# Kernel optimization log

Hardware: AMD Instinct MI355X
Metric: run time of the kernel (lower is better)

Reference implementation:

```python
import jax, jax.numpy as jnp
import numpy as np

T, B, E, H = 2048, 2, 1024, 16
HD = E // H
EPS = 1e-5


def setup_inputs() -> dict:
    key = jax.random.key(0)
    k1, k2, k3 = jax.random.split(key, 3)
    bound_in = float(np.sqrt(6.0 / (3 * E + E)))   # xavier_uniform for [3E,E]
    bound_out = float(np.sqrt(6.0 / (E + E)))      # xavier_uniform for [E,E]
    return {
        "query": jax.random.normal(k1, (T, B, E), dtype=jnp.float32),
        "gamma": jnp.ones((E,), dtype=jnp.float32),
        "beta": jnp.zeros((E,), dtype=jnp.float32),
        "in_proj_weight": jax.random.uniform(k2, (3 * E, E), jnp.float32, -bound_in, bound_in),
        "out_proj_weight": jax.random.uniform(k3, (E, E), jnp.float32, -bound_out, bound_out),
    }


def reference(query, gamma, beta, in_proj_weight, out_proj_weight):
    # LayerNorm over channel dim
    mean = jnp.mean(query, axis=-1, keepdims=True)
    var = jnp.mean(jnp.square(query - mean), axis=-1, keepdims=True)
    ln = (query - mean) * jax.lax.rsqrt(var + EPS) * gamma + beta  # [T,B,E]

    # Fused QKV projection (no bias): qkv = ln @ W^T, W: [3E, E]
    qkv = jnp.einsum("tbe,fe->tbf", ln, in_proj_weight)  # [T,B,3E]
    q, k, v = jnp.split(qkv, 3, axis=-1)
    q = q.reshape(T, B, H, HD) * (HD ** -0.5)
    k = k.reshape(T, B, H, HD)
    v = v.reshape(T, B, H, HD)

    # Attention: scores [B,H,T,T]
    scores = jnp.einsum("tbhd,sbhd->bhts", q, k)
    attn = jax.nn.softmax(scores, axis=-1)
    ctx = jnp.einsum("bhts,sbhd->tbhd", attn, v).reshape(T, B, E)

    # Output projection + residual add (dropout prob = 0)
    out = jnp.einsum("tbe,fe->tbf", ctx, out_proj_weight)
    return query + out
```

## Files before the change

### kernel.cpp

```cpp
#include <hip/hip_runtime.h>
#include <hip/hip_bf16.h>
#include <math.h>

#define T_DIM 2048
#define B_DIM 2
#define E_DIM 1024
#define H_DIM 16
#define HD_DIM 64
#define M_DIM (T_DIM * B_DIM)
#define BH_DIM (B_DIM * H_DIM)

using bf16x8 = __attribute__((ext_vector_type(8))) __bf16;
using u16x8  = __attribute__((ext_vector_type(8))) unsigned short;
using f32x4  = __attribute__((ext_vector_type(4))) float;

static __device__ __forceinline__ unsigned short f2bf(float f) {
  unsigned u = __builtin_bit_cast(unsigned, f);
  u += 0x7fff + ((u >> 16) & 1);
  return (unsigned short)(u >> 16);
}

__device__ __forceinline__ void gload_lds16(const void* g, void* l) {
  __builtin_amdgcn_global_load_lds(
      (const __attribute__((address_space(1))) unsigned int*)g,
      (__attribute__((address_space(3))) unsigned int*)l, 16, 0, 0);
}

__global__ __launch_bounds__(256) void prep_kernel(
    const float* __restrict__ q, const float* __restrict__ gamma,
    const float* __restrict__ beta, unsigned short* __restrict__ ln_out,
    const float* __restrict__ w1, unsigned short* __restrict__ o1, int n1,
    const float* __restrict__ w2, unsigned short* __restrict__ o2, int n2) {
  int blk = blockIdx.x;
  int tid = threadIdx.x;
  if (blk >= M_DIM) {
    int i = (blk - M_DIM) * 256 + tid;
    const float* in; unsigned short* out; int idx;
    if (i < n1) { in = w1; out = o1; idx = i; }
    else if (i < n1 + n2) { in = w2; out = o2; idx = i - n1; }
    else return;
    float4 v = ((const float4*)in)[idx];
    ushort4 o;
    o.x = f2bf(v.x); o.y = f2bf(v.y); o.z = f2bf(v.z); o.w = f2bf(v.w);
    ((ushort4*)out)[idx] = o;
    return;
  }
  int row = blk;
  const float4* qr = (const float4*)(q + (size_t)row * E_DIM);
  float4 x = qr[tid];
  float s  = x.x + x.y + x.z + x.w;
  float ss = x.x * x.x + x.y * x.y + x.z * x.z + x.w * x.w;
#pragma unroll
  for (int off = 32; off >= 1; off >>= 1) {
    s  += __shfl_xor(s, off, 64);
    ss += __shfl_xor(ss, off, 64);
  }
  __shared__ float red[8];
  int wid = tid >> 6, lane = tid & 63;
  if (lane == 0) { red[wid] = s; red[4 + wid] = ss; }
  __syncthreads();
  s  = red[0] + red[1] + red[2] + red[3];
  ss = red[4] + red[5] + red[6] + red[7];
  float mean = s * (1.0f / E_DIM);
  float var  = ss * (1.0f / E_DIM) - mean * mean;
  float rstd = rsqrtf(var + 1e-5f);
  float4 g4 = ((const float4*)gamma)[tid];
  float4 b4 = ((const float4*)beta)[tid];
  ushort4 o;
  o.x = f2bf((x.x - mean) * rstd * g4.x + b4.x);
  o.y = f2bf((x.y - mean) * rstd * g4.y + b4.y);
  o.z = f2bf((x.z - mean) * rstd * g4.z + b4.z);
  o.w = f2bf((x.w - mean) * rstd * g4.w + b4.w);
  ((ushort4*)(ln_out + (size_t)row * E_DIM))[tid] = o;
}

__global__ __launch_bounds__(256) void gemm0_kernel(
    const unsigned short* __restrict__ A, const unsigned short* __restrict__ Bw,
    unsigned short* __restrict__ out_qkv) {
  __shared__ alignas(16) unsigned short lA[3][128 * 32];
  __shared__ alignas(16) unsigned short lB[3][128 * 32];
  int tid = threadIdx.x;
  int wid = tid >> 6, lane = tid & 63;
  int wm = wid >> 1, wn = wid & 1;
  int g = lane >> 4, lr = lane & 15;
  int m0 = blockIdx.y * 128, n0 = blockIdx.x * 128;
  f32x4 acc[4][4] = {};

#define STAGE_G0(BUF, K0)                                                      \
  do {                                                                         \
    _Pragma("unroll")                                                          \
    for (int c = 0; c < 2; ++c) {                                              \
      int f16 = c * 256 + tid;                                                 \
      int row = f16 >> 2, col8 = (f16 & 3) << 3;                               \
      gload_lds16(A  + (size_t)(m0 + row) * E_DIM + (K0) + col8,               \
                  lA[BUF] + (size_t)(c * 256 + wid * 64) * 8);                 \
      gload_lds16(Bw + (size_t)(n0 + row) * E_DIM + (K0) + col8,               \
                  lB[BUF] + (size_t)(c * 256 + wid * 64) * 8);                 \
    }                                                                          \
  } while (0)

#define PROCG0(BUF, NBUF, KK, LAST)                                            \
  do {                                                                         \
    if (!(LAST)) {                                                             \
      STAGE_G0(NBUF, ((KK) + 1) * 32);                                         \
      asm volatile("s_waitcnt vmcnt(4)" ::: "memory");                         \
    } else {                                                                   \
      asm volatile("s_waitcnt vmcnt(0)" ::: "memory");                         \
    }                                                                          \
    __builtin_amdgcn_s_barrier();                                              \
    __builtin_amdgcn_sched_barrier(0);                                         \
    bf16x8 af[4], bfr[4];                                                      \
    _Pragma("unroll")                                                          \
    for (int r = 0; r < 4; ++r) {                                              \
      af[r]  = *(const bf16x8*)(lA[BUF] + (wm * 64 + r * 16 + lr) * 32 + g * 8); \
      bfr[r] = *(const bf16x8*)(lB[BUF] + (wn * 64 + r * 16 + lr) * 32 + g * 8); \
    }                                                                          \
    __builtin_amdgcn_s_setprio(1);                                             \
    _Pragma("unroll")                                                          \
    for (int mr = 0; mr < 4; ++mr)                                             \
      _Pragma("unroll")                                                        \
      for (int nr = 0; nr < 4; ++nr)                                           \
        acc[mr][nr] = __builtin_amdgcn_mfma_f32_16x16x32_bf16(                 \
            af[mr], bfr[nr], acc[mr][nr], 0, 0, 0);                            \
    __builtin_amdgcn_s_setprio(0);                                             \
  } while (0)

  STAGE_G0(0, 0);
  for (int kk = 0; kk < 30; kk += 3) {
    PROCG0(0, 1, kk + 0, false);
    PROCG0(1, 2, kk + 1, false);
    PROCG0(2, 0, kk + 2, false);
  }
  PROCG0(0, 1, 30, false);
  PROCG0(1, 2, 31, true);
#undef PROCG0
#undef STAGE_G0

#pragma unroll
  for (int mr = 0; mr < 4; ++mr) {
#pragma unroll
    for (int nr = 0; nr < 4; ++nr) {
#pragma unroll
      for (int r = 0; r < 4; ++r) {
        int grow = m0 + wm * 64 + mr * 16 + g * 4 + r;
        int gcol = n0 + wn * 64 + nr * 16 + lr;
        int which = gcol >> 10, rem = gcol & 1023;
        int h = rem >> 6, d = rem & 63;
        int t = grow >> 1, b = grow & 1;
        out_qkv[(size_t)which * (BH_DIM * T_DIM * HD_DIM) +
                ((size_t)(b * H_DIM + h) * T_DIM + t) * HD_DIM + d] =
            f2bf(acc[mr][nr][r]);
      }
    }
  }
}

__global__ __launch_bounds__(256) void gemm1_kernel(
    const unsigned short* __restrict__ A, const unsigned short* __restrict__ Bw,
    const float* __restrict__ resid, float* __restrict__ out) {
  __shared__ alignas(16) unsigned short lA[3][128 * 32];
  __shared__ alignas(16) unsigned short lB[3][64 * 32];
  int tid = threadIdx.x;
  int wid = tid >> 6, lane = tid & 63;
  int g = lane >> 4, lr = lane & 15;
  int m0 = blockIdx.y * 128, n0 = blockIdx.x * 64;
  f32x4 acc[2][4] = {};

#define STAGE_G1(BUF, K0)                                                      \
  do {                                                                         \
    _Pragma("unroll")                                                          \
    for (int c = 0; c < 2; ++c) {                                              \
      int f16 = c * 256 + tid;                                                 \
      int row = f16 >> 2, col8 = (f16 & 3) << 3;                               \
      gload_lds16(A + (size_t)(m0 + row) * E_DIM + (K0) + col8,                \
                  lA[BUF] + (size_t)(c * 256 + wid * 64) * 8);                 \
    }                                                                          \
    {                                                                          \
      int row = tid >> 2, col8 = (tid & 3) << 3;                               \
      gload_lds16(Bw + (size_t)(n0 + row) * E_DIM + (K0) + col8,               \
                  lB[BUF] + (size_t)(wid * 64) * 8);                           \
    }                                                                          \
  } while (0)

#define PROCG1(BUF, NBUF, KK, LAST)                                            \
  do {                                                                         \
    if (!(LAST)) {                                                             \
      STAGE_G1(NBUF, ((KK) + 1) * 32);                                         \
      asm volatile("s_waitcnt vmcnt(3)" ::: "memory");                         \
    } else {                                                                   \
      asm volatile("s_waitcnt vmcnt(0)" ::: "memory");                         \
    }                                                                          \
    __builtin_amdgcn_s_barrier();                                              \
    __builtin_amdgcn_sched_barrier(0);                                         \
    bf16x8 af[2], bfr[4];                                                      \
    _Pragma("unroll")                                                          \
    for (int r = 0; r < 2; ++r)                                                \
      af[r] = *(const bf16x8*)(lA[BUF] + (wid * 32 + r * 16 + lr) * 32 + g * 8); \
    _Pragma("unroll")                                                          \
    for (int r = 0; r < 4; ++r)                                                \
      bfr[r] = *(const bf16x8*)(lB[BUF] + (r * 16 + lr) * 32 + g * 8);         \
    __builtin_amdgcn_s_setprio(1);                                             \
    _Pragma("unroll")                                                          \
    for (int mr = 0; mr < 2; ++mr)                                             \
      _Pragma("unroll")                                                        \
      for (int nr = 0; nr < 4; ++nr)                                           \
        acc[mr][nr] = __builtin_amdgcn_mfma_f32_16x16x32_bf16(                 \
            af[mr], bfr[nr], acc[mr][nr], 0, 0, 0);                            \
    __builtin_amdgcn_s_setprio(0);                                             \
  } while (0)

  STAGE_G1(0, 0);
  for (int kk = 0; kk < 30; kk += 3) {
    PROCG1(0, 1, kk + 0, false);
    PROCG1(1, 2, kk + 1, false);
    PROCG1(2, 0, kk + 2, false);
  }
  PROCG1(0, 1, 30, false);
  PROCG1(1, 2, 31, true);
#undef PROCG1
#undef STAGE_G1

#pragma unroll
  for (int mr = 0; mr < 2; ++mr) {
#pragma unroll
    for (int nr = 0; nr < 4; ++nr) {
#pragma unroll
      for (int r = 0; r < 4; ++r) {
        int grow = m0 + wid * 32 + mr * 16 + g * 4 + r;
        int gcol = n0 + nr * 16 + lr;
        size_t idx = (size_t)grow * E_DIM + gcol;
        out[idx] = resid[idx] + acc[mr][nr][r];
      }
    }
  }
}

__global__ __launch_bounds__(256) void transpose_v_kernel(
    const unsigned short* __restrict__ vb, unsigned short* __restrict__ vt) {
  __shared__ alignas(16) unsigned short tl[64 * 72];
  int tid = threadIdx.x;
  int bh = blockIdx.y, t0 = blockIdx.x * 64;
  const unsigned short* src = vb + ((size_t)bh * T_DIM + t0) * HD_DIM;
#pragma unroll
  for (int e = 0; e < 2; ++e) {
    int i8 = e * 256 + tid;
    int r = i8 >> 3;
    int c = (i8 & 7) * 8;
    int hsh = (r ^ (r >> 3)) & 7;
    bf16x8 v = *(const bf16x8*)(src + (size_t)r * HD_DIM + c);
    *(bf16x8*)(tl + r * 72 + (c ^ (hsh << 3))) = v;
  }
  __syncthreads();
  unsigned short* dst = vt + (size_t)bh * HD_DIM * T_DIM + t0;
#pragma unroll
  for (int e = 0; e < 2; ++e) {
    int i8 = e * 256 + tid;
    int d = i8 >> 3;
    int tc = (i8 & 7) * 8;
    u16x8 o;
#pragma unroll
    for (int j = 0; j < 8; ++j) {
      int p = tc + j;
      int ks = p >> 5, gg = (p >> 3) & 3, jl = p & 7;
      int r = (ks * 2 + (jl >> 2)) * 16 + gg * 4 + (jl & 3);
      int hsh = (r ^ (r >> 3)) & 7;
      o[j] = tl[r * 72 + (d ^ (hsh << 3))];
    }
    *(u16x8*)(dst + (size_t)d * T_DIM + tc) = o;
  }
}

__global__ __launch_bounds__(256) void attn_kernel(
    const unsigned short* __restrict__ qb, const unsigned short* __restrict__ kb,
    const unsigned short* __restrict__ vt, unsigned short* __restrict__ ctx) {
  __shared__ alignas(16) unsigned short lK[4][64 * 64];
  __shared__ alignas(16) unsigned short lV[4][64 * 64];
  int tid = threadIdx.x;
  int wid = tid >> 6, lane = tid & 63;
  int g = lane >> 4, lr = lane & 15;
  int f = blockIdx.x;
  int xcd = f & 7, rest = f >> 3;
  int bh = xcd + 8 * (rest & 3);
  int qt = rest >> 2;
  int b = bh >> 4, h = bh & 15;
  const size_t koff = (size_t)bh * T_DIM * HD_DIM;
  const size_t voff = (size_t)bh * HD_DIM * T_DIM;

  int srow = tid >> 3;
  int gch  = (tid & 7) ^ (srow & 7);
  const unsigned short* ks0 = kb + koff + (size_t)srow * HD_DIM + gch * 8;
  const unsigned short* vs0 = vt + voff + (size_t)srow * T_DIM + gch * 8;

#define STAGE_TILE(buf, T)                                                     \
  do {                                                                         \
    size_t kofs = (size_t)(T) * 64 * HD_DIM;                                   \
    size_t vofs = (size_t)(T) * 64;                                            \
    gload_lds16(ks0 + kofs,                 lK[buf] + wid * 512);              \
    gload_lds16(ks0 + kofs + 32 * HD_DIM,   lK[buf] + 2048 + wid * 512);       \
    gload_lds16(vs0 + vofs,                 lV[buf] + wid * 512);              \
    gload_lds16(vs0 + vofs + (size_t)32 * T_DIM, lV[buf] + 2048 + wid * 512);  \
  } while (0)

  bf16x8 qf[2][2];
  {
    const float QS = 0.125f * 1.44269504f;
#pragma unroll
    for (int qa = 0; qa < 2; ++qa) {
      int qrow = qt * 128 + wid * 32 + qa * 16 + lr;
#pragma unroll
      for (int ks = 0; ks < 2; ++ks) {
        bf16x8 raw = *(const bf16x8*)(qb + koff + (size_t)qrow * HD_DIM + ks * 32 + g * 8);
#pragma unroll
        for (int j = 0; j < 8; ++j) qf[qa][ks][j] = (__bf16)((float)raw[j] * QS);
      }
    }
  }

  bf16x8 onesf;
#pragma unroll
  for (int j = 0; j < 8; ++j) onesf[j] = (__bf16)1.0f;

  f32x4 accO[2][4] = {};
  f32x4 accS[2] = {};

#define COMPUTE_TILE(B)                                                        \
  do {                                                                         \
    const unsigned short* Kc = lK[B];                                          \
    const unsigned short* Vc = lV[B];                                          \
    f32x4 s4[2][4];                                                            \
    __builtin_amdgcn_s_setprio(1);                                             \
    _Pragma("unroll")                                                          \
    for (int cf = 0; cf < 4; ++cf) {                                           \
      int row = cf * 16 + lr;                                                  \
      int sw = (row & 7) << 3;                                                 \
      bf16x8 k0 = *(const bf16x8*)(Kc + row * 64 + ((g * 8) ^ sw));            \
      bf16x8 k1 = *(const bf16x8*)(Kc + row * 64 + ((32 + g * 8) ^ sw));       \
      _Pragma("unroll")                                                        \
      for (int qa = 0; qa < 2; ++qa) {                                         \
        f32x4 s = {-8.0f, -8.0f, -8.0f, -8.0f};                                \
        s = __builtin_amdgcn_mfma_f32_16x16x32_bf16(k0, qf[qa][0], s, 0, 0, 0);\
        s = __builtin_amdgcn_mfma_f32_16x16x32_bf16(k1, qf[qa][1], s, 0, 0, 0);\
        s4[qa][cf] = s;                                                        \
      }                                                                        \
    }                                                                          \
    __builtin_amdgcn_s_setprio(0);                                             \
    bf16x8 pf[2][2];                                                           \
    _Pragma("unroll")                                                          \
    for (int qa = 0; qa < 2; ++qa)                                             \
      _Pragma("unroll")                                                        \
      for (int j = 0; j < 8; ++j) {                                            \
        pf[qa][0][j] = (__bf16)__builtin_amdgcn_exp2f(s4[qa][(j >> 2)][j & 3]);\
        pf[qa][1][j] = (__bf16)__builtin_amdgcn_exp2f(s4[qa][2 + (j >> 2)][j & 3]);\
      }                                                                        \
    __builtin_amdgcn_s_setprio(1);                                             \
    _Pragma("unroll")                                                          \
    for (int ks = 0; ks < 2; ++ks) {                                           \
      _Pragma("unroll")                                                        \
      for (int qa = 0; qa < 2; ++qa)                                           \
        accS[qa] = __builtin_amdgcn_mfma_f32_16x16x32_bf16(onesf, pf[qa][ks], accS[qa], 0, 0, 0); \
      _Pragma("unroll")                                                        \
      for (int df = 0; df < 4; ++df) {                                         \
        int row = df * 16 + lr;                                                \
        int sw = (row & 7) << 3;                                               \
        bf16x8 vf = *(const bf16x8*)(Vc + row * 64 + ((ks * 32 + g * 8) ^ sw));\
        _Pragma("unroll")                                                      \
        for (int qa = 0; qa < 2; ++qa)                                         \
          accO[qa][df] = __builtin_amdgcn_mfma_f32_16x16x32_bf16(vf, pf[qa][ks], accO[qa][df], 0, 0, 0); \
      }                                                                        \
    }                                                                          \
    __builtin_amdgcn_s_setprio(0);                                             \
  } while (0)

#define INTERVAL(BA, BB, SA, SB, TT, STG)                                      \
  do {                                                                         \
    asm volatile("s_waitcnt vmcnt(0)" ::: "memory");                           \
    __builtin_amdgcn_s_barrier();                                              \
    __builtin_amdgcn_sched_barrier(0);                                         \
    if (STG) {                                                                 \
      STAGE_TILE(SA, (TT) + 2);                                                \
      STAGE_TILE(SB, (TT) + 3);                                                \
    }                                                                          \
    COMPUTE_TILE(BA);                                                          \
    COMPUTE_TILE(BB);                                                          \
  } while (0)

  STAGE_TILE(0, 0);
  STAGE_TILE(1, 1);
  for (int tt = 0; tt < 28; tt += 4) {
    INTERVAL(0, 1, 2, 3, tt, true);
    INTERVAL(2, 3, 0, 1, tt + 2, true);
  }
  INTERVAL(0, 1, 2, 3, 28, true);
  INTERVAL(2, 3, 0, 1, 30, false);
#undef INTERVAL
#undef COMPUTE_TILE
#undef STAGE_TILE

  __syncthreads();
  unsigned short* sc = (unsigned short*)lK + wid * (32 * 72);
  float invl[2];
  invl[0] = 1.0f / accS[0][0];
  invl[1] = 1.0f / accS[1][0];
#pragma unroll
  for (int qa = 0; qa < 2; ++qa)
#pragma unroll
    for (int df = 0; df < 4; ++df)
#pragma unroll
      for (int r = 0; r < 4; ++r)
        sc[(qa * 16 + lr) * 72 + df * 16 + g * 4 + r] =
            f2bf(accO[qa][df][r] * invl[qa]);
  __syncthreads();
#pragma unroll
  for (int i = 0; i < 4; ++i) {
    int idx = i * 64 + lane;
    int row = idx >> 3, ch = idx & 7;
    u16x8 v8 = *(const u16x8*)(sc + row * 72 + ch * 8);
    int t = qt * 128 + wid * 32 + row;
    *(u16x8*)(&ctx[((size_t)t * B_DIM + b) * E_DIM + h * HD_DIM + ch * 8]) = v8;
  }
}

extern "C" void kernel_launch(void* const* d_in, const int* in_sizes, int n_in,
                              void* d_out, int out_size, void* d_ws, size_t ws_size,
                              hipStream_t stream) {
  const float* query = (const float*)d_in[0];
  const float* gamma = (const float*)d_in[1];
  const float* beta  = (const float*)d_in[2];
  const float* w_in  = (const float*)d_in[3];
  const float* w_out = (const float*)d_in[4];
  float* out = (float*)d_out;

  unsigned short* ws    = (unsigned short*)d_ws;
  unsigned short* ln    = ws;
  unsigned short* winb  = ln + (size_t)M_DIM * E_DIM;
  unsigned short* woutb = winb + (size_t)3 * E_DIM * E_DIM;
  unsigned short* qkv   = woutb + (size_t)E_DIM * E_DIM;

  unsigned short* qbuf = qkv;
  unsigned short* kbuf = qkv + (size_t)BH_DIM * T_DIM * HD_DIM;
  unsigned short* vbuf = kbuf + (size_t)BH_DIM * T_DIM * HD_DIM;
  unsigned short* vtb  = ln;
  unsigned short* ctx  = vbuf;

  prep_kernel<<<dim3(M_DIM + 4096), dim3(256), 0, stream>>>(
      query, gamma, beta, ln,
      w_in, winb, 3 * E_DIM * E_DIM / 4, w_out, woutb, E_DIM * E_DIM / 4);
  gemm0_kernel<<<dim3(3 * E_DIM / 128, M_DIM / 128), dim3(256), 0, stream>>>(
      ln, winb, qkv);
  transpose_v_kernel<<<dim3(T_DIM / 64, BH_DIM), dim3(256), 0, stream>>>(vbuf, vtb);
  attn_kernel<<<dim3(512), dim3(256), 0, stream>>>(qbuf, kbuf, vtb, ctx);
  gemm1_kernel<<<dim3(E_DIM / 64, M_DIM / 128), dim3(256), 0, stream>>>(
      ctx, woutb, query, out);
}
```

Before: 122.2 us.

## Fuse V transpose into QKV GEMM epilogue via shared-memory staging

The QKV projection kernel now writes Q and K directly and, for V column blocks, stages the accumulator tile in shared memory and writes V already in the transposed, MFMA-permuted layout the attention kernel expects. This removes the separate transpose kernel launch and the round trip of V through global memory. In exchange the V blocks pay an extra barrier and scalar LDS gathers with a padded stride, and the workspace layout is reshuffled so ctx reuses the LN buffer.

```diff
diff --git a/kernel.cpp b/kernel.cpp
--- a/kernel.cpp
+++ b/kernel.cpp
@@ -76,14 +76,17 @@
 
 __global__ __launch_bounds__(256) void gemm0_kernel(
     const unsigned short* __restrict__ A, const unsigned short* __restrict__ Bw,
-    unsigned short* __restrict__ out_qkv) {
-  __shared__ alignas(16) unsigned short lA[3][128 * 32];
-  __shared__ alignas(16) unsigned short lB[3][128 * 32];
+    unsigned short* __restrict__ out_q, unsigned short* __restrict__ out_k,
+    unsigned short* __restrict__ out_vt) {
+  __shared__ alignas(16) unsigned short smem[24576];
+#define LA(BUF) (smem + (size_t)(BUF) * 4096)
+#define LB(BUF) (smem + 12288 + (size_t)(BUF) * 4096)
   int tid = threadIdx.x;
   int wid = tid >> 6, lane = tid & 63;
   int wm = wid >> 1, wn = wid & 1;
   int g = lane >> 4, lr = lane & 15;
-  int m0 = blockIdx.y * 128, n0 = blockIdx.x * 128;
+  int bx = blockIdx.x, by = blockIdx.y;
+  int m0 = by * 128, n0 = bx * 128;
   f32x4 acc[4][4] = {};
 
 #define STAGE_G0(BUF, K0)                                                      \
@@ -93,9 +96,9 @@
       int f16 = c * 256 + tid;                                                 \
       int row = f16 >> 2, col8 = (f16 & 3) << 3;                               \
       gload_lds16(A  + (size_t)(m0 + row) * E_DIM + (K0) + col8,               \
-                  lA[BUF] + (size_t)(c * 256 + wid * 64) * 8);                 \
+                  LA(BUF) + (size_t)(c * 256 + wid * 64) * 8);                 \
       gload_lds16(Bw + (size_t)(n0 + row) * E_DIM + (K0) + col8,               \
-                  lB[BUF] + (size_t)(c * 256 + wid * 64) * 8);                 \
+                  LB(BUF) + (size_t)(c * 256 + wid * 64) * 8);                 \
     }                                                                          \
   } while (0)
 
@@ -112,8 +115,8 @@
     bf16x8 af[4], bfr[4];                                                      \
     _Pragma("unroll")                                                          \
     for (int r = 0; r < 4; ++r) {                                              \
-      af[r]  = *(const bf16x8*)(lA[BUF] + (wm * 64 + r * 16 + lr) * 32 + g * 8); \
-      bfr[r] = *(const bf16x8*)(lB[BUF] + (wn * 64 + r * 16 + lr) * 32 + g * 8); \
+      af[r]  = *(const bf16x8*)(LA(BUF) + (wm * 64 + r * 16 + lr) * 32 + g * 8); \
+      bfr[r] = *(const bf16x8*)(LB(BUF) + (wn * 64 + r * 16 + lr) * 32 + g * 8); \
     }                                                                          \
     __builtin_amdgcn_s_setprio(1);                                             \
     _Pragma("unroll")                                                          \
@@ -135,21 +138,63 @@
   PROCG0(1, 2, 31, true);
 #undef PROCG0
 #undef STAGE_G0
-
-#pragma unroll
-  for (int mr = 0; mr < 4; ++mr) {
-#pragma unroll
-    for (int nr = 0; nr < 4; ++nr) {
-#pragma unroll
-      for (int r = 0; r < 4; ++r) {
-        int grow = m0 + wm * 64 + mr * 16 + g * 4 + r;
-        int gcol = n0 + wn * 64 + nr * 16 + lr;
-        int which = gcol >> 10, rem = gcol & 1023;
-        int h = rem >> 6, d = rem & 63;
-        int t = grow >> 1, b = grow & 1;
-        out_qkv[(size_t)which * (BH_DIM * T_DIM * HD_DIM) +
-                ((size_t)(b * H_DIM + h) * T_DIM + t) * HD_DIM + d] =
-            f2bf(acc[mr][nr][r]);
+#undef LA
+#undef LB
+
+  if (bx < 16) {
+    unsigned short* outp = (bx < 8) ? out_q : out_k;
+#pragma unroll
+    for (int mr = 0; mr < 4; ++mr) {
+#pragma unroll
+      for (int nr = 0; nr < 4; ++nr) {
+#pragma unroll
+        for (int r = 0; r < 4; ++r) {
+          int grow = m0 + wm * 64 + mr * 16 + g * 4 + r;
+          int gcol = n0 + wn * 64 + nr * 16 + lr;
+          int rem = gcol & 1023;
+          int h = rem >> 6, d = rem & 63;
+          int t = grow >> 1, b = grow & 1;
+          outp[((size_t)(b * H_DIM + h) * T_DIM + t) * HD_DIM + d] =
+              f2bf(acc[mr][nr][r]);
+        }
+      }
+    }
+  } else {
+    __syncthreads();
+    unsigned short* tbuf = smem;
+#pragma unroll
+    for (int mr = 0; mr < 4; ++mr)
+#pragma unroll
+      for (int nr = 0; nr < 4; ++nr)
+#pragma unroll
+        for (int r = 0; r < 4; ++r) {
+          int rowl = wm * 64 + mr * 16 + g * 4 + r;
+          int coll = wn * 64 + nr * 16 + lr;
+          tbuf[rowl * 137 + coll] = f2bf(acc[mr][nr][r]);
+        }
+    __syncthreads();
+    int hbase = (bx - 16) * 2;
+#pragma unroll
+    for (int bb = 0; bb < 2; ++bb) {
+#pragma unroll
+      for (int hh = 0; hh < 2; ++hh) {
+        size_t bhv = (size_t)(bb * H_DIM + hbase + hh);
+        unsigned short* dst = out_vt + bhv * ((size_t)HD_DIM * T_DIM) + by * 64;
+#pragma unroll
+        for (int e = 0; e < 2; ++e) {
+          int i8 = e * 256 + tid;
+          int d = i8 >> 3;
+          int tc = (i8 & 7) * 8;
+          u16x8 o;
+#pragma unroll
+          for (int j = 0; j < 8; ++j) {
+            int p = tc + j;
+            int ks = p >> 5, gg = (p >> 3) & 3, jl = p & 7;
+            int tl = (ks * 2 + (jl >> 2)) * 16 + gg * 4 + (jl & 3);
+            o[j] = tbuf[(2 * tl + bb) * 137 + hh * 64 + d];
+          }
+          *(u16x8*)(dst + (size_t)d * T_DIM + tc) = o;
+        }
       }
     }
   }
@@ -232,41 +277,6 @@
         out[idx] = resid[idx] + acc[mr][nr][r];
       }
     }
-  }
-}
-
-__global__ __launch_bounds__(256) void transpose_v_kernel(
-    const unsigned short* __restrict__ vb, unsigned short* __restrict__ vt) {
-  __shared__ alignas(16) unsigned short tl[64 * 72];
-  int tid = threadIdx.x;
-  int bh = blockIdx.y, t0 = blockIdx.x * 64;
-  const unsigned short* src = vb + ((size_t)bh * T_DIM + t0) * HD_DIM;
-#pragma unroll
-  for (int e = 0; e < 2; ++e) {
-    int i8 = e * 256 + tid;
-    int r = i8 >> 3;
-    int c = (i8 & 7) * 8;
-    int hsh = (r ^ (r >> 3)) & 7;
-    bf16x8 v = *(const bf16x8*)(src + (size_t)r * HD_DIM + c);
-    *(bf16x8*)(tl + r * 72 + (c ^ (hsh << 3))) = v;
-  }
-  __syncthreads();
-  unsigned short* dst = vt + (size_t)bh * HD_DIM * T_DIM + t0;
-#pragma unroll
-  for (int e = 0; e < 2; ++e) {
-    int i8 = e * 256 + tid;
-    int d = i8 >> 3;
-    int tc = (i8 & 7) * 8;
-    u16x8 o;
-#pragma unroll
-    for (int j = 0; j < 8; ++j) {
-      int p = tc + j;
-      int ks = p >> 5, gg = (p >> 3) & 3, jl = p & 7;
-      int r = (ks * 2 + (jl >> 2)) * 16 + gg * 4 + (jl & 3);
-      int hsh = (r ^ (r >> 3)) & 7;
-      o[j] = tl[r * 72 + (d ^ (hsh << 3))];
-    }
-    *(u16x8*)(dst + (size_t)d * T_DIM + tc) = o;
   }
 }
 
@@ -432,22 +442,18 @@
 
   unsigned short* ws    = (unsigned short*)d_ws;
   unsigned short* ln    = ws;
-  unsigned short* winb  = ln + (size_t)M_DIM * E_DIM;
-  unsigned short* woutb = winb + (size_t)3 * E_DIM * E_DIM;
-  unsigned short* qkv   = woutb + (size_t)E_DIM * E_DIM;
-
-  unsigned short* qbuf = qkv;
-  unsigned short* kbuf = qkv + (size_t)BH_DIM * T_DIM * HD_DIM;
-  unsigned short* vbuf = kbuf + (size_t)BH_DIM * T_DIM * HD_DIM;
-  unsigned short* vtb  = ln;
-  unsigned short* ctx  = vbuf;
+  unsigned short* winb  = ln    + (size_t)M_DIM * E_DIM;
+  unsigned short* woutb = winb  + (size_t)3 * E_DIM * E_DIM;
+  unsigned short* qbuf  = woutb + (size_t)E_DIM * E_DIM;
+  unsigned short* kbuf  = qbuf  + (size_t)BH_DIM * T_DIM * HD_DIM;
+  unsigned short* vtb   = kbuf  + (size_t)BH_DIM * T_DIM * HD_DIM;
+  unsigned short* ctx   = ln;
 
   prep_kernel<<<dim3(M_DIM + 4096), dim3(256), 0, stream>>>(
       query, gamma, beta, ln,
       w_in, winb, 3 * E_DIM * E_DIM / 4, w_out, woutb, E_DIM * E_DIM / 4);
   gemm0_kernel<<<dim3(3 * E_DIM / 128, M_DIM / 128), dim3(256), 0, stream>>>(
-      ln, winb, qkv);
-  transpose_v_kernel<<<dim3(T_DIM / 64, BH_DIM), dim3(256), 0, stream>>>(vbuf, vtb);
+      ln, winb, qbuf, kbuf, vtb);
   attn_kernel<<<dim3(512), dim3(256), 0, stream>>>(qbuf, kbuf, vtb, ctx);
   gemm1_kernel<<<dim3(E_DIM / 64, M_DIM / 128), dim3(256), 0, stream>>>(
       ctx, woutb, query, out);
```

After: 122.4 us. No clear change (+0.2%).
